# Performance work log

Hardware: AMD Instinct MI355X
Metric: run time of the kernel (lower is better)

## Reference

```python
import jax, jax.numpy as jnp
import numpy as np

SEQ_LENS = [1024, 768, 512, 896, 640, 384, 1024, 896]
TOTAL = sum(SEQ_LENS)  # 6144
EMBED = 768
NUM_HEADS = 12
HEAD_DIM = EMBED // NUM_HEADS
FFN = 3072
LN_EPS = 1e-5


def _pad_maps():
    # static (numpy) index maps for ragged <-> padded layout
    B, S = len(SEQ_LENS), max(SEQ_LENS)
    offs = np.cumsum([0] + SEQ_LENS)
    pad_idx = np.zeros((B, S), np.int32)
    valid = np.zeros((B, S), bool)
    for i, L in enumerate(SEQ_LENS):
        pad_idx[i, :L] = np.arange(offs[i], offs[i] + L)
        valid[i, :L] = True
    flat_b = np.concatenate([np.full(L, i, np.int32) for i, L in enumerate(SEQ_LENS)])
    flat_p = np.concatenate([np.arange(L, dtype=np.int32) for L in SEQ_LENS])
    return jnp.asarray(pad_idx), jnp.asarray(valid), jnp.asarray(flat_b), jnp.asarray(flat_p)

PAD_IDX, VALID, FLAT_B, FLAT_P = _pad_maps()


def _layernorm(x, g, b):
    mu = jnp.mean(x, axis=-1, keepdims=True)
    var = jnp.mean(jnp.square(x - mu), axis=-1, keepdims=True)
    return (x - mu) * jax.lax.rsqrt(var + LN_EPS) * g + b


def setup_inputs() -> dict:
    key = jax.random.key(0)
    ks = jax.random.split(key, 8)
    return {
        "hidden_states": jax.random.normal(ks[0], (TOTAL, EMBED), jnp.float32),
        "attention_mask": jnp.ones((TOTAL,), jnp.int32),
        "in_proj_w": 0.02 * jax.random.normal(ks[1], (3 * EMBED, EMBED), jnp.float32),
        "in_proj_b": jnp.zeros((3 * EMBED,), jnp.float32),
        "out_proj_w": 0.02 * jax.random.normal(ks[2], (EMBED, EMBED), jnp.float32),
        "out_proj_b": jnp.zeros((EMBED,), jnp.float32),
        "ln1_g": jnp.ones((EMBED,), jnp.float32),
        "ln1_b": jnp.zeros((EMBED,), jnp.float32),
        "fc1_w": 0.02 * jax.random.normal(ks[3], (FFN, EMBED), jnp.float32),
        "fc1_b": jnp.zeros((FFN,), jnp.float32),
        "fc2_w": 0.02 * jax.random.normal(ks[4], (EMBED, FFN), jnp.float32),
        "fc2_b": jnp.zeros((EMBED,), jnp.float32),
        "ln2_g": jnp.ones((EMBED,), jnp.float32),
        "ln2_b": jnp.zeros((EMBED,), jnp.float32),
    }


def reference(hidden_states, attention_mask, in_proj_w, in_proj_b, out_proj_w,
              out_proj_b, ln1_g, ln1_b, fc1_w, fc1_b, fc2_w, fc2_b, ln2_g, ln2_b):
    B, S = PAD_IDX.shape
    residual = hidden_states
    x = _layernorm(hidden_states, ln1_g, ln1_b)  # pre-LN (do_layer_norm_before)

    # ragged -> padded [B, S, E]; key validity combines padding mask and ragged tail
    xp = x[PAD_IDX]
    key_valid = VALID & (attention_mask[PAD_IDX] != 0)

    # fused QKV projection (nn.MultiheadAttention in_proj)
    qkv = xp @ in_proj_w.T + in_proj_b  # [B, S, 3E]
    q, k, v = jnp.split(qkv, 3, axis=-1)
    q = q.reshape(B, S, NUM_HEADS, HEAD_DIM) * (1.0 / np.sqrt(HEAD_DIM))
    k = k.reshape(B, S, NUM_HEADS, HEAD_DIM)
    v = v.reshape(B, S, NUM_HEADS, HEAD_DIM)

    scores = jnp.einsum('bqhd,bkhd->bhqk', q, k)  # [B, H, S, S]
    causal = jnp.tril(jnp.ones((S, S), bool))
    mask = causal[None, None] & key_valid[:, None, None, :]
    scores = jnp.where(mask, scores, jnp.float32(-1e30))
    probs = jax.nn.softmax(scores, axis=-1)
    ctx = jnp.einsum('bhqk,bkhd->bqhd', probs, v).reshape(B, S, EMBED)
    attn = ctx @ out_proj_w.T + out_proj_b

    # padded -> ragged, residual
    h = residual + attn[FLAT_B, FLAT_P]

    # FFN block (pre-LN)
    residual = h
    h = _layernorm(h, ln2_g, ln2_b)
    h = jax.nn.relu(h @ fc1_w.T + fc1_b)
    h = h @ fc2_w.T + fc2_b
    return residual + h
```

## Files before the change

### kernel.cpp

```cpp
#include <hip/hip_runtime.h>
#include <hip/hip_bf16.h>

#define TOTAL 6144
#define EMBED 768
#define QKV3  2304
#define FFN   3072
#define NH    12
#define HD    64
#define NSEG  412
#define NCQT  128
#define SLOTB 4608

typedef unsigned short u16;
typedef unsigned int u32;
typedef float f32x4 __attribute__((ext_vector_type(4)));
typedef __bf16 bf16x8 __attribute__((ext_vector_type(8)));

__device__ __constant__ int BOFF[9] = {0, 1024, 1792, 2304, 3200, 3840, 4224, 5248, 6144};

struct SegT {
    short segstart[193];
    short qt_of_seg[NSEG];
    short cqt[NCQT];
};
constexpr SegT make_segt() {
    SegT s{};
    const int toff[9] = {0, 32, 56, 72, 100, 120, 132, 164, 192};
    int tot = 0, cc = 0;
    for (int qt = 0; qt < 192; ++qt) {
        int b = 0;
        for (int i = 0; i < 8; ++i)
            if (qt >= toff[i + 1]) b = i + 1;
        int t = qt - toff[b];
        int nch = t / 2 + 1;
        int ns = (nch + 3) / 4;
        s.segstart[qt] = (short)tot;
        for (int j = 0; j < ns; ++j) s.qt_of_seg[tot + j] = (short)qt;
        tot += ns;
        if (ns >= 2) s.cqt[cc++] = (short)qt;
    }
    s.segstart[192] = (short)tot;
    return s;
}
__device__ __constant__ SegT SEGT = make_segt();

__device__ __forceinline__ u16 f2b(float f) {
    __bf16 h = (__bf16)f;
    return __builtin_bit_cast(u16, h);
}
__device__ __forceinline__ float b2f(u16 h) {
    union { u32 u; float f; } v; v.u = ((u32)h) << 16; return v.f;
}

__device__ __forceinline__ void gload_lds16(const u16* g, u16* l) {
    __builtin_amdgcn_global_load_lds(
        (const __attribute__((address_space(1))) u32*)(uintptr_t)g,
        (__attribute__((address_space(3))) u32*)(uintptr_t)l, 16, 0, 0);
}

__device__ __forceinline__ float rowmax16(float x) {
    int v;
    v = __builtin_amdgcn_mov_dpp(__float_as_int(x), 0xB1, 0xF, 0xF, true);
    x = fmaxf(x, __int_as_float(v));
    v = __builtin_amdgcn_mov_dpp(__float_as_int(x), 0x4E, 0xF, 0xF, true);
    x = fmaxf(x, __int_as_float(v));
    v = __builtin_amdgcn_mov_dpp(__float_as_int(x), 0x124, 0xF, 0xF, true);
    x = fmaxf(x, __int_as_float(v));
    v = __builtin_amdgcn_mov_dpp(__float_as_int(x), 0x128, 0xF, 0xF, true);
    x = fmaxf(x, __int_as_float(v));
    return x;
}

__global__ void cvt4m_kernel(const float* __restrict__ s0, u16* __restrict__ d0, int n0,
                             const float* __restrict__ s1, u16* __restrict__ d1, int n1,
                             const float* __restrict__ s2, u16* __restrict__ d2, int n2,
                             const float* __restrict__ s3, u16* __restrict__ d3, int n3,
                             const int* __restrict__ am, u32* __restrict__ mb) {
    if (blockIdx.x >= 6912) {
        int g = (blockIdx.x - 6912) * 4 + (threadIdx.x >> 6);
        int lane = threadIdx.x & 63;
        unsigned long long bal = __ballot(am[g * 64 + lane] != 0);
        if (lane == 0) {
            mb[g * 2] = (u32)bal;
            mb[g * 2 + 1] = (u32)(bal >> 32);
        }
        return;
    }
    int i = blockIdx.x * blockDim.x + threadIdx.x;
    const float* s;
    u16* d;
    int j = i;
    if (j < n0) { s = s0; d = d0; }
    else {
        j -= n0;
        if (j < n1) { s = s1; d = d1; }
        else {
            j -= n1;
            if (j < n2) { s = s2; d = d2; }
            else {
                j -= n2;
                if (j >= n3) return;
                s = s3; d = d3;
            }
        }
    }
    float4 v = ((const float4*)s)[j];
    ushort4 o;
    o.x = f2b(v.x); o.y = f2b(v.y); o.z = f2b(v.z); o.w = f2b(v.w);
    ((ushort4*)d)[j] = o;
}

__global__ __launch_bounds__(256) void ln_kernel(const float* __restrict__ x,
                                                 const float* __restrict__ g,
                                                 const float* __restrict__ b,
                                                 u16* __restrict__ out) {
    int row = blockIdx.x * 4 + (threadIdx.x >> 6);
    int lane = threadIdx.x & 63;
    const float* xr = x + (size_t)row * EMBED;
    float4 v[3];
    float s = 0.f, sq = 0.f;
#pragma unroll
    for (int c = 0; c < 3; ++c) {
        v[c] = *(const float4*)(xr + c * 256 + lane * 4);
        s += v[c].x + v[c].y + v[c].z + v[c].w;
        sq += v[c].x * v[c].x + v[c].y * v[c].y + v[c].z * v[c].z + v[c].w * v[c].w;
    }
#pragma unroll
    for (int o = 32; o; o >>= 1) {
        s += __shfl_xor(s, o);
        sq += __shfl_xor(sq, o);
    }
    float mu = s * (1.f / 768.f);
    float var = sq * (1.f / 768.f) - mu * mu;
    float rs = rsqrtf(var + 1e-5f);
    u16* orow = out + (size_t)row * EMBED;
#pragma unroll
    for (int c = 0; c < 3; ++c) {
        int col = c * 256 + lane * 4;
        float4 gg = *(const float4*)(g + col);
        float4 bb = *(const float4*)(b + col);
        ushort4 o;
        o.x = f2b((v[c].x - mu) * rs * gg.x + bb.x);
        o.y = f2b((v[c].y - mu) * rs * gg.y + bb.y);
        o.z = f2b((v[c].z - mu) * rs * gg.z + bb.z);
        o.w = f2b((v[c].w - mu) * rs * gg.w + bb.w);
        *(ushort4*)(orow + col) = o;
    }
}

template <int RELU, int RES, int OUTB, int OUTF, int VTR>
__global__ __launch_bounds__(256) void gemm128(const u16* __restrict__ A,
                                               const u16* __restrict__ B,
                                               const float* __restrict__ bias,
                                               const float* __restrict__ res,
                                               u16* __restrict__ outb,
                                               float* __restrict__ outf,
                                               u16* __restrict__ vout,
                                               int M, int N, int K) {
    __shared__ u16 As[2][128][64];
    __shared__ u16 Bs[2][128][64];
    int t = threadIdx.x;
    int lane = t & 63, w = t >> 6;
    int wr = w >> 1, wc = w & 1;
    int gx = gridDim.x;
    int nwg = gx * gridDim.y;
    int flat = blockIdx.y * gx + blockIdx.x;
    int swz = (flat & 7) * (nwg >> 3) + (flat >> 3);
    int m0 = (swz / gx) * 128, n0 = (swz % gx) * 128;
    int lr = lane >> 3;
    int lcg = (lane & 7) ^ (lr & 7);
    int c16 = lane & 15, hi = lane >> 4;

    f32x4 acc[4][4];
#pragma unroll
    for (int m = 0; m < 4; ++m)
#pragma unroll
        for (int n = 0; n < 4; ++n) acc[m][n] = (f32x4)0.f;

    const u16* Ab = A + (size_t)(m0 + w * 32 + lr) * K + lcg * 8;
    const u16* Bb = B + (size_t)(n0 + w * 32 + lr) * K + lcg * 8;

    int nk = K >> 6;
#pragma unroll
    for (int i = 0; i < 4; ++i) {
        gload_lds16(Ab + (size_t)(i * 8) * K, &As[0][w * 32 + i * 8][0]);
        gload_lds16(Bb + (size_t)(i * 8) * K, &Bs[0][w * 32 + i * 8][0]);
    }

    for (int tk = 0; tk < nk; ++tk) {
        int cur = tk & 1;
        if (tk + 1 < nk) {
            int k1 = (tk + 1) << 6;
#pragma unroll
            for (int i = 0; i < 4; ++i) {
                gload_lds16(Ab + (size_t)(i * 8) * K + k1, &As[cur ^ 1][w * 32 + i * 8][0]);
                gload_lds16(Bb + (size_t)(i * 8) * K + k1, &Bs[cur ^ 1][w * 32 + i * 8][0]);
            }
            asm volatile("s_waitcnt vmcnt(8)" ::: "memory");
        } else {
            asm volatile("s_waitcnt vmcnt(0)" ::: "memory");
        }
        __builtin_amdgcn_sched_barrier(0);
        __builtin_amdgcn_s_barrier();
#pragma unroll
        for (int ks = 0; ks < 2; ++ks) {
            bf16x8 af[4], bfr[4];
#pragma unroll
            for (int m = 0; m < 4; ++m)
                af[m] = *(const bf16x8*)&As[cur][wr * 64 + m * 16 + c16][((ks * 4 + hi) ^ (c16 & 7)) * 8];
#pragma unroll
            for (int n = 0; n < 4; ++n)
                bfr[n] = *(const bf16x8*)&Bs[cur][wc * 64 + n * 16 + c16][((ks * 4 + hi) ^ (c16 & 7)) * 8];
#pragma unroll
            for (int m = 0; m < 4; ++m)
#pragma unroll
                for (int n = 0; n < 4; ++n)
                    acc[m][n] = __builtin_amdgcn_mfma_f32_16x16x32_bf16(af[m], bfr[n], acc[m][n], 0, 0, 0);
        }
        asm volatile("s_waitcnt lgkmcnt(0)" ::: "memory");
        __builtin_amdgcn_sched_barrier(0);
        __builtin_amdgcn_s_barrier();
    }

#pragma unroll
    for (int m = 0; m < 4; ++m)
#pragma unroll
        for (int n = 0; n < 4; ++n) {
            int cg = n0 + wc * 64 + n * 16 + c16;
            float bv = bias[cg];
            float vj[4];
#pragma unroll
            for (int j = 0; j < 4; ++j) {
                int rg = m0 + wr * 64 + m * 16 + hi * 4 + j;
                float v = acc[m][n][j] + bv;
                if (RELU) v = fmaxf(v, 0.f);
                if (RES) v += res[(size_t)rg * N + cg];
                vj[j] = v;
                if (OUTB) outb[(size_t)rg * N + cg] = f2b(v);
                if (OUTF) outf[(size_t)rg * N + cg] = v;
            }
            if (VTR && cg >= 2 * EMBED) {
                ushort4 tv;
                tv.x = f2b(vj[0]); tv.y = f2b(vj[1]); tv.z = f2b(vj[2]); tv.w = f2b(vj[3]);
                int rgb = m0 + wr * 64 + m * 16 + hi * 4;
                *(ushort4*)&vout[(size_t)(cg - 2 * EMBED) * TOTAL + rgb] = tv;
            }
        }
}

__global__ __launch_bounds__(64, 2) void attn_mfma(const u16* __restrict__ qkv,
                                                   const u16* __restrict__ vT,
                                                   const u32* __restrict__ mbits,
                                                   u16* __restrict__ ctx,
                                                   char* __restrict__ pbuf) {
    __shared__ u16 Pl[32][64];
    int l = threadIdx.x;
    int hi = l >> 4, c = l & 15;
    int bidg = blockIdx.x;
    int swz = (bidg & 7) * (NSEG * NH / 8) + (bidg >> 3);
    int h = swz / NSEG;
    int sl = swz % NSEG;
    int qt = SEGT.qt_of_seg[sl];
    int seg = sl - SEGT.segstart[qt];
    int nseg = SEGT.segstart[qt + 1] - SEGT.segstart[qt];
    int r0 = qt * 32;
    int b = 0;
#pragma unroll
    for (int i = 0; i < 8; ++i)
        if (r0 >= BOFF[i + 1]) b = i + 1;
    int boff = BOFF[b];
    int p0 = r0 - boff;
    int nchunks = (p0 >> 6) + 1;
    int nfull = (p0 >= 63) ? (((p0 - 63) >> 6) + 1) : 0;
    int kc0 = seg * 4;
    int kc1 = min(kc0 + 4, nchunks);
    const float SCALE = 0.125f * 1.44269504f;

    bf16x8 qa[2][2];
#pragma unroll
    for (int m = 0; m < 2; ++m)
#pragma unroll
        for (int ks = 0; ks < 2; ++ks)
            qa[m][ks] = *(const bf16x8*)&qkv[(size_t)(r0 + m * 16 + c) * QKV3 + h * HD + ks * 32 + hi * 8];

    bf16x8 vones;
#pragma unroll
    for (int j = 0; j < 8; ++j) vones[j] = (__bf16)1.0f;

    f32x4 oacc[2][4], lacc[2];
    float mrun[2][4];
#pragma unroll
    for (int m = 0; m < 2; ++m) {
        lacc[m] = (f32x4)0.f;
#pragma unroll
        for (int nt = 0; nt < 4; ++nt) oacc[m][nt] = (f32x4)0.f;
#pragma unroll
        for (int r = 0; r < 4; ++r) mrun[m][r] = -1e30f;
    }

    for (int kc = kc0; kc < kc1; ++kc) {
        int k0 = kc << 6;
        bf16x8 kb[2][4], vb[2][4];
#pragma unroll
        for (int ks = 0; ks < 2; ++ks)
#pragma unroll
            for (int nt = 0; nt < 4; ++nt) {
                kb[ks][nt] = *(const bf16x8*)&qkv[(size_t)(boff + k0 + nt * 16 + c) * QKV3 +
                                                  EMBED + h * HD + ks * 32 + hi * 8];
                vb[ks][nt] = *(const bf16x8*)&vT[(size_t)(h * HD + nt * 16 + c) * TOTAL +
                                                 boff + k0 + ks * 32 + hi * 8];
            }
        int wi = (boff + k0) >> 5;
        u32 mw0 = mbits[wi], mw1 = mbits[wi + 1];

        f32x4 sacc[2][4];
#pragma unroll
        for (int m = 0; m < 2; ++m)
#pragma unroll
            for (int nt = 0; nt < 4; ++nt) sacc[m][nt] = (f32x4)0.f;
        __builtin_amdgcn_s_setprio(1);
#pragma unroll
        for (int ks = 0; ks < 2; ++ks)
#pragma unroll
            for (int m = 0; m < 2; ++m)
#pragma unroll
                for (int nt = 0; nt < 4; ++nt)
                    sacc[m][nt] = __builtin_amdgcn_mfma_f32_16x16x32_bf16(qa[m][ks], kb[ks][nt], sacc[m][nt], 0, 0, 0);
        __builtin_amdgcn_s_setprio(0);

        bool fullmask = ((mw0 & mw1) == 0xFFFFFFFFu);
        if (kc >= nfull) {
#pragma unroll
            for (int m = 0; m < 2; ++m)
#pragma unroll
                for (int nt = 0; nt < 4; ++nt) {
                    int kpos = k0 + nt * 16 + c;
                    u32 mwv = (nt & 2) ? mw1 : mw0;
                    float madd = fullmask ? 0.f
                        : (((mwv >> (((nt & 1) << 4) + c)) & 1u) ? 0.f : -1e30f);
#pragma unroll
                    for (int r = 0; r < 4; ++r) {
                        int qp = p0 + m * 16 + 4 * hi + r;
                        sacc[m][nt][r] = (kpos <= qp) ? (sacc[m][nt][r] + madd) : -1e30f;
                    }
                }
        } else if (!fullmask) {
#pragma unroll
            for (int m = 0; m < 2; ++m)
#pragma unroll
                for (int nt = 0; nt < 4; ++nt) {
                    u32 mwv = (nt & 2) ? mw1 : mw0;
                    float madd = ((mwv >> (((nt & 1) << 4) + c)) & 1u) ? 0.f : -1e30f;
#pragma unroll
                    for (int r = 0; r < 4; ++r) sacc[m][nt][r] += madd;
                }
        }

        float mx[2][4];
        int small = 1;
#pragma unroll
        for (int m = 0; m < 2; ++m)
#pragma unroll
            for (int r = 0; r < 4; ++r) {
                float v = fmaxf(fmaxf(sacc[m][0][r], sacc[m][1][r]),
                                fmaxf(sacc[m][2][r], sacc[m][3][r]));
                v = rowmax16(v);
                mx[m][r] = v;
                small &= (v <= mrun[m][r]) ? 1 : 0;
            }
        if (!__all(small)) {
#pragma unroll
            for (int m = 0; m < 2; ++m)
#pragma unroll
                for (int r = 0; r < 4; ++r) {
                    float mn = fmaxf(mrun[m][r], mx[m][r]);
                    float f = exp2f((mrun[m][r] - mn) * SCALE);
                    mrun[m][r] = mn;
                    lacc[m][r] *= f;
#pragma unroll
                    for (int nt = 0; nt < 4; ++nt) oacc[m][nt][r] *= f;
                }
        }

        float negm[2][4];
#pragma unroll
        for (int m = 0; m < 2; ++m)
#pragma unroll
            for (int r = 0; r < 4; ++r) negm[m][r] = -mrun[m][r] * SCALE;
#pragma unroll
        for (int m = 0; m < 2; ++m)
#pragma unroll
            for (int nt = 0; nt < 4; ++nt)
#pragma unroll
                for (int r = 0; r < 4; ++r) {
                    float p = exp2f(fmaf(sacc[m][nt][r], SCALE, negm[m][r]));
                    int row = m * 16 + 4 * hi + r;
                    int cch = ((nt * 2 + (c >> 3)) ^ (row & 7)) << 3;
                    Pl[row][cch + (c & 7)] = f2b(p);
                }

#pragma unroll
        for (int ks = 0; ks < 2; ++ks) {
            bf16x8 pa[2];
#pragma unroll
            for (int m = 0; m < 2; ++m)
                pa[m] = *(const bf16x8*)&Pl[m * 16 + c][(((ks * 4 + hi) ^ (c & 7)) << 3)];
            __builtin_amdgcn_s_setprio(1);
#pragma unroll
            for (int m = 0; m < 2; ++m) {
                lacc[m] = __builtin_amdgcn_mfma_f32_16x16x32_bf16(pa[m], vones, lacc[m], 0, 0, 0);
#pragma unroll
                for (int nt = 0; nt < 4; ++nt)
                    oacc[m][nt] = __builtin_amdgcn_mfma_f32_16x16x32_bf16(pa[m], vb[ks][nt], oacc[m][nt], 0, 0, 0);
            }
            __builtin_amdgcn_s_setprio(0);
        }
    }

    if (nseg == 1) {
#pragma unroll
        for (int m = 0; m < 2; ++m)
#pragma unroll
            for (int r = 0; r < 4; ++r) {
                float inv = 1.0f / lacc[m][r];
#pragma unroll
                for (int nt = 0; nt < 4; ++nt)
                    ctx[(size_t)(r0 + m * 16 + 4 * hi + r) * EMBED + h * HD + nt * 16 + c] =
                        f2b(oacc[m][nt][r] * inv);
            }
    } else {
        char* base = pbuf + (size_t)(h * NSEG + sl) * SLOTB;
        u16* Op = (u16*)base;
        float* mlp = (float*)(base + 4096);
#pragma unroll
        for (int m = 0; m < 2; ++m)
#pragma unroll
            for (int r = 0; r < 4; ++r) {
                int row = m * 16 + 4 * hi + r;
                float inv = 1.0f / lacc[m][r];
#pragma unroll
                for (int nt = 0; nt < 4; ++nt)
                    Op[row * 64 + nt * 16 + c] = f2b(oacc[m][nt][r] * inv);
                if (c == 0) {
                    mlp[row * 2] = mrun[m][r];
                    mlp[row * 2 + 1] = lacc[m][r];
                }
            }
    }
}

__global__ __launch_bounds__(256) void attn_combine(const char* __restrict__ pbuf,
                                                    u16* __restrict__ ctx) {
    int cid = blockIdx.x;
    int h = cid % NH;
    int qt = SEGT.cqt[cid / NH];
    int s0 = SEGT.segstart[qt];
    int ns = SEGT.segstart[qt + 1] - s0;
    int t = threadIdx.x;
    int r = t >> 3;
    int cg = t & 7;
    int r0 = qt * 32;
    const float SCALE = 0.125f * 1.44269504f;

    float mj[4], lj[4];
    uint4 ov[4];
#pragma unroll
    for (int j = 0; j < 4; ++j) {
        const char* base = pbuf + (size_t)(h * NSEG + s0 + min(j, ns - 1)) * SLOTB;
        float2 ml = *(const float2*)(base + 4096 + r * 8);
        mj[j] = (j < ns) ? ml.x : -1e30f;
        lj[j] = (j < ns) ? ml.y : 0.f;
        ov[j] = *(const uint4*)(base + (r * 64 + cg * 8) * 2);
    }
    float M = fmaxf(fmaxf(mj[0], mj[1]), fmaxf(mj[2], mj[3]));
    float e[4], wsum = 0.f;
#pragma unroll
    for (int j = 0; j < 4; ++j) {
        e[j] = (j < ns) ? exp2f((mj[j] - M) * SCALE) * lj[j] : 0.f;
        wsum += e[j];
    }
    float inv = 1.0f / wsum;
    u16 outv[8];
#pragma unroll
    for (int k = 0; k < 8; ++k) {
        float o = 0.f;
#pragma unroll
        for (int j = 0; j < 4; ++j)
            o += e[j] * b2f(((const u16*)&ov[j])[k]);
        outv[k] = f2b(o * inv);
    }
    *(uint4*)&ctx[(size_t)(r0 + r) * EMBED + h * HD + cg * 8] = *(uint4*)outv;
}

extern "C" void kernel_launch(void* const* d_in, const int* in_sizes, int n_in,
                              void* d_out, int out_size, void* d_ws, size_t ws_size,
                              hipStream_t stream) {
    (void)in_sizes; (void)n_in; (void)out_size; (void)ws_size;
    const float* hidden = (const float*)d_in[0];
    const int*   amask  = (const int*)d_in[1];
    const float* in_w   = (const float*)d_in[2];
    const float* in_b   = (const float*)d_in[3];
    const float* out_w  = (const float*)d_in[4];
    const float* out_b  = (const float*)d_in[5];
    const float* ln1g   = (const float*)d_in[6];
    const float* ln1b   = (const float*)d_in[7];
    const float* fc1w   = (const float*)d_in[8];
    const float* fc1b   = (const float*)d_in[9];
    const float* fc2w   = (const float*)d_in[10];
    const float* fc2b   = (const float*)d_in[11];
    const float* ln2g   = (const float*)d_in[12];
    const float* ln2b   = (const float*)d_in[13];
    float* out = (float*)d_out;

    char* ws = (char*)d_ws;
    size_t off = 0;
    auto alloc = [&](size_t bytes) {
        void* p = ws + off;
        off += (bytes + 255) & ~(size_t)255;
        return p;
    };
    u16* w_in_bf  = (u16*)alloc((size_t)QKV3 * EMBED * 2);
    u16* w_out_bf = (u16*)alloc((size_t)EMBED * EMBED * 2);
    u16* w_fc1_bf = (u16*)alloc((size_t)FFN * EMBED * 2);
    u16* w_fc2_bf = (u16*)alloc((size_t)EMBED * FFN * 2);
    u16* xln  = (u16*)alloc((size_t)TOTAL * EMBED * 2);
    u16* qkv  = (u16*)alloc((size_t)TOTAL * QKV3 * 2);
    u16* ctx  = (u16*)alloc((size_t)TOTAL * EMBED * 2);
    float* hmid = (float*)alloc((size_t)TOTAL * EMBED * 4);
    u16* hln  = (u16*)alloc((size_t)TOTAL * EMBED * 2);
    u16* f1o  = (u16*)alloc((size_t)TOTAL * FFN * 2);
    u32* mbits = (u32*)alloc(192 * 4);
    u16* vT = hln;
    char* pbuf = (char*)f1o;

    cvt4m_kernel<<<6936, 256, 0, stream>>>(in_w, w_in_bf, 442368,
                                           out_w, w_out_bf, 147456,
                                           fc1w, w_fc1_bf, 589824,
                                           fc2w, w_fc2_bf, 589824,
                                           amask, mbits);

    ln_kernel<<<TOTAL / 4, 256, 0, stream>>>(hidden, ln1g, ln1b, xln);
    gemm128<0, 0, 1, 0, 1><<<dim3(QKV3 / 128, TOTAL / 128), 256, 0, stream>>>(
        xln, w_in_bf, in_b, nullptr, qkv, nullptr, vT, TOTAL, QKV3, EMBED);
    attn_mfma<<<dim3(NSEG * NH), 64, 0, stream>>>(qkv, vT, mbits, ctx, pbuf);
    attn_combine<<<dim3(NCQT * NH), 256, 0, stream>>>(pbuf, ctx);
    gemm128<0, 1, 0, 1, 0><<<dim3(EMBED / 128, TOTAL / 128), 256, 0, stream>>>(
        ctx, w_out_bf, out_b, hidden, nullptr, hmid, nullptr, TOTAL, EMBED, EMBED);
    ln_kernel<<<TOTAL / 4, 256, 0, stream>>>(hmid, ln2g, ln2b, hln);
    gemm128<1, 0, 1, 0, 0><<<dim3(FFN / 128, TOTAL / 128), 256, 0, stream>>>(
        hln, w_fc1_bf, fc1b, nullptr, f1o, nullptr, nullptr, TOTAL, FFN, EMBED);
    gemm128<0, 1, 0, 1, 0><<<dim3(EMBED / 128, TOTAL / 128), 256, 0, stream>>>(
        f1o, w_fc2_bf, fc2b, hmid, nullptr, out, nullptr, TOTAL, EMBED, FFN);
}
```

Measured before the change: 214.6 us.

## Add 3-stage GEMM pipeline for FC2 and pack four attention segments per block

The GEMM gains a STAGES template parameter. A 3-deep LDS ring buffer with adjusted vmcnt waits is enabled only for the long-K FC2 projection, to hide more global-load latency. Separately, the attention kernel now runs four independent 64-lane segments per 256-thread workgroup, each with its own P tile in LDS, and uses a per-XCD block remapping. This cuts the number of workgroups, but raises LDS use per block. The FC2 occupancy may drop because the 3-stage buffers need 96KB of LDS per block.

```diff
diff --git a/kernel.cpp b/kernel.cpp
--- a/kernel.cpp
+++ b/kernel.cpp
@@ -148,7 +148,7 @@
     }
 }
 
-template <int RELU, int RES, int OUTB, int OUTF, int VTR>
+template <int RELU, int RES, int OUTB, int OUTF, int VTR, int STAGES>
 __global__ __launch_bounds__(256) void gemm128(const u16* __restrict__ A,
                                                const u16* __restrict__ B,
                                                const float* __restrict__ bias,
@@ -157,8 +157,8 @@
                                                float* __restrict__ outf,
                                                u16* __restrict__ vout,
                                                int M, int N, int K) {
-    __shared__ u16 As[2][128][64];
-    __shared__ u16 Bs[2][128][64];
+    __shared__ u16 As[STAGES][128][64];
+    __shared__ u16 Bs[STAGES][128][64];
     int t = threadIdx.x;
     int lane = t & 63, w = t >> 6;
     int wr = w >> 1, wc = w & 1;
@@ -181,24 +181,28 @@
     const u16* Bb = B + (size_t)(n0 + w * 32 + lr) * K + lcg * 8;
 
     int nk = K >> 6;
-#pragma unroll
-    for (int i = 0; i < 4; ++i) {
-        gload_lds16(Ab + (size_t)(i * 8) * K, &As[0][w * 32 + i * 8][0]);
-        gload_lds16(Bb + (size_t)(i * 8) * K, &Bs[0][w * 32 + i * 8][0]);
-    }
+    auto issue = [&](int tk, int buf) {
+        int k0 = tk << 6;
+#pragma unroll
+        for (int i = 0; i < 4; ++i) {
+            gload_lds16(Ab + (size_t)(i * 8) * K + k0, &As[buf][w * 32 + i * 8][0]);
+            gload_lds16(Bb + (size_t)(i * 8) * K + k0, &Bs[buf][w * 32 + i * 8][0]);
+        }
+    };
+    issue(0, 0);
+    if (STAGES == 3 && nk > 1) issue(1, 1);
 
     for (int tk = 0; tk < nk; ++tk) {
-        int cur = tk & 1;
-        if (tk + 1 < nk) {
-            int k1 = (tk + 1) << 6;
-#pragma unroll
-            for (int i = 0; i < 4; ++i) {
-                gload_lds16(Ab + (size_t)(i * 8) * K + k1, &As[cur ^ 1][w * 32 + i * 8][0]);
-                gload_lds16(Bb + (size_t)(i * 8) * K + k1, &Bs[cur ^ 1][w * 32 + i * 8][0]);
-            }
-            asm volatile("s_waitcnt vmcnt(8)" ::: "memory");
+        int cur = (STAGES == 2) ? (tk & 1) : (tk % 3);
+        if (tk + STAGES - 1 < nk)
+            issue(tk + STAGES - 1, (STAGES == 2) ? (cur ^ 1) : ((tk + 2) % 3));
+        if (STAGES == 3) {
+            if (tk + 2 < nk)      asm volatile("s_waitcnt vmcnt(16)" ::: "memory");
+            else if (tk + 1 < nk) asm volatile("s_waitcnt vmcnt(8)" ::: "memory");
+            else                  asm volatile("s_waitcnt vmcnt(0)" ::: "memory");
         } else {
-            asm volatile("s_waitcnt vmcnt(0)" ::: "memory");
+            if (tk + 1 < nk)      asm volatile("s_waitcnt vmcnt(8)" ::: "memory");
+            else                  asm volatile("s_waitcnt vmcnt(0)" ::: "memory");
         }
         __builtin_amdgcn_sched_barrier(0);
         __builtin_amdgcn_s_barrier();
@@ -248,18 +252,21 @@
         }
 }
 
-__global__ __launch_bounds__(64, 2) void attn_mfma(const u16* __restrict__ qkv,
-                                                   const u16* __restrict__ vT,
-                                                   const u32* __restrict__ mbits,
-                                                   u16* __restrict__ ctx,
-                                                   char* __restrict__ pbuf) {
-    __shared__ u16 Pl[32][64];
-    int l = threadIdx.x;
+__global__ __launch_bounds__(256) void attn_mfma(const u16* __restrict__ qkv,
+                                                 const u16* __restrict__ vT,
+                                                 const u32* __restrict__ mbits,
+                                                 u16* __restrict__ ctx,
+                                                 char* __restrict__ pbuf) {
+    __shared__ u16 Pl[4][32][64];
+    int l = threadIdx.x & 63, w = threadIdx.x >> 6;
     int hi = l >> 4, c = l & 15;
-    int bidg = blockIdx.x;
-    int swz = (bidg & 7) * (NSEG * NH / 8) + (bidg >> 3);
-    int h = swz / NSEG;
-    int sl = swz % NSEG;
+    int bid = blockIdx.x;
+    int xcd = bid & 7;
+    int base = (xcd < 4) ? xcd * 155 : 4 * 155 + (xcd - 4) * 154;
+    int wgid = base + (bid >> 3);
+    int sidx = wgid * 4 + w;
+    int h = sidx / NSEG;
+    int sl = sidx % NSEG;
     int qt = SEGT.qt_of_seg[sl];
     int seg = sl - SEGT.segstart[qt];
     int nseg = SEGT.segstart[qt + 1] - SEGT.segstart[qt];
@@ -396,7 +403,7 @@
                     float p = exp2f(fmaf(sacc[m][nt][r], SCALE, negm[m][r]));
                     int row = m * 16 + 4 * hi + r;
                     int cch = ((nt * 2 + (c >> 3)) ^ (row & 7)) << 3;
-                    Pl[row][cch + (c & 7)] = f2b(p);
+                    Pl[w][row][cch + (c & 7)] = f2b(p);
                 }
 
 #pragma unroll
@@ -404,7 +411,7 @@
             bf16x8 pa[2];
 #pragma unroll
             for (int m = 0; m < 2; ++m)
-                pa[m] = *(const bf16x8*)&Pl[m * 16 + c][(((ks * 4 + hi) ^ (c & 7)) << 3)];
+                pa[m] = *(const bf16x8*)&Pl[w][m * 16 + c][(((ks * 4 + hi) ^ (c & 7)) << 3)];
             __builtin_amdgcn_s_setprio(1);
 #pragma unroll
             for (int m = 0; m < 2; ++m) {
@@ -429,9 +436,9 @@
                         f2b(oacc[m][nt][r] * inv);
             }
     } else {
-        char* base = pbuf + (size_t)(h * NSEG + sl) * SLOTB;
-        u16* Op = (u16*)base;
-        float* mlp = (float*)(base + 4096);
+        char* base2 = pbuf + (size_t)(h * NSEG + sl) * SLOTB;
+        u16* Op = (u16*)base2;
+        float* mlp = (float*)(base2 + 4096);
 #pragma unroll
         for (int m = 0; m < 2; ++m)
 #pragma unroll
@@ -540,15 +547,15 @@
                                            amask, mbits);
 
     ln_kernel<<<TOTAL / 4, 256, 0, stream>>>(hidden, ln1g, ln1b, xln);
-    gemm128<0, 0, 1, 0, 1><<<dim3(QKV3 / 128, TOTAL / 128), 256, 0, stream>>>(
+    gemm128<0, 0, 1, 0, 1, 2><<<dim3(QKV3 / 128, TOTAL / 128), 256, 0, stream>>>(
         xln, w_in_bf, in_b, nullptr, qkv, nullptr, vT, TOTAL, QKV3, EMBED);
-    attn_mfma<<<dim3(NSEG * NH), 64, 0, stream>>>(qkv, vT, mbits, ctx, pbuf);
+    attn_mfma<<<dim3(NSEG * NH / 4), 256, 0, stream>>>(qkv, vT, mbits, ctx, pbuf);
     attn_combine<<<dim3(NCQT * NH), 256, 0, stream>>>(pbuf, ctx);
-    gemm128<0, 1, 0, 1, 0><<<dim3(EMBED / 128, TOTAL / 128), 256, 0, stream>>>(
+    gemm128<0, 1, 0, 1, 0, 2><<<dim3(EMBED / 128, TOTAL / 128), 256, 0, stream>>>(
         ctx, w_out_bf, out_b, hidden, nullptr, hmid, nullptr, TOTAL, EMBED, EMBED);
     ln_kernel<<<TOTAL / 4, 256, 0, stream>>>(hmid, ln2g, ln2b, hln);
-    gemm128<1, 0, 1, 0, 0><<<dim3(FFN / 128, TOTAL / 128), 256, 0, stream>>>(
+    gemm128<1, 0, 1, 0, 0, 2><<<dim3(FFN / 128, TOTAL / 128), 256, 0, stream>>>(
         hln, w_fc1_bf, fc1b, nullptr, f1o, nullptr, nullptr, TOTAL, FFN, EMBED);
-    gemm128<0, 1, 0, 1, 0><<<dim3(EMBED / 128, TOTAL / 128), 256, 0, stream>>>(
+    gemm128<0, 1, 0, 1, 0, 3><<<dim3(EMBED / 128, TOTAL / 128), 256, 0, stream>>>(
         f1o, w_fc2_bf, fc2b, hmid, nullptr, out, nullptr, TOTAL, EMBED, FFN);
 }
```

New measurement: 270.9 us. +26.3%, slower.

## Split FC2 GEMM K dimension in two with separate partial-sum add kernel

Applied to the files above, without the earlier changes.

The FC2 GEMM is launched with twice the workgroups, each covering half of K. The second half writes raw partial sums into the dead qkv buffer, and a new elementwise kernel adds them into the output. This targets the poor wave fill of the 288-block grid on a 256-CU device, at the cost of an extra fp32 write/read pass and one more kernel launch.

```diff
diff --git a/kernel.cpp b/kernel.cpp
--- a/kernel.cpp
+++ b/kernel.cpp
@@ -148,7 +148,7 @@
     }
 }
 
-template <int RELU, int RES, int OUTB, int OUTF, int VTR>
+template <int RELU, int RES, int OUTB, int OUTF, int VTR, int SPLITK>
 __global__ __launch_bounds__(256) void gemm128(const u16* __restrict__ A,
                                                const u16* __restrict__ B,
                                                const float* __restrict__ bias,
@@ -156,6 +156,7 @@
                                                u16* __restrict__ outb,
                                                float* __restrict__ outf,
                                                u16* __restrict__ vout,
+                                               float* __restrict__ outf2,
                                                int M, int N, int K) {
     __shared__ u16 As[2][128][64];
     __shared__ u16 Bs[2][128][64];
@@ -166,7 +167,12 @@
     int nwg = gx * gridDim.y;
     int flat = blockIdx.y * gx + blockIdx.x;
     int swz = (flat & 7) * (nwg >> 3) + (flat >> 3);
-    int m0 = (swz / gx) * 128, n0 = (swz % gx) * 128;
+    int cx = swz % gx;
+    int nxt = gx / SPLITK;
+    int kh = (SPLITK > 1) ? (cx / nxt) : 0;
+    int n0 = (cx % nxt) * 128;
+    int m0 = (swz / gx) * 128;
+    int Ksub = K / SPLITK;
     int lr = lane >> 3;
     int lcg = (lane & 7) ^ (lr & 7);
     int c16 = lane & 15, hi = lane >> 4;
@@ -177,10 +183,10 @@
 #pragma unroll
         for (int n = 0; n < 4; ++n) acc[m][n] = (f32x4)0.f;
 
-    const u16* Ab = A + (size_t)(m0 + w * 32 + lr) * K + lcg * 8;
-    const u16* Bb = B + (size_t)(n0 + w * 32 + lr) * K + lcg * 8;
-
-    int nk = K >> 6;
+    const u16* Ab = A + (size_t)(m0 + w * 32 + lr) * K + kh * Ksub + lcg * 8;
+    const u16* Bb = B + (size_t)(n0 + w * 32 + lr) * K + kh * Ksub + lcg * 8;
+
+    int nk = Ksub >> 6;
 #pragma unroll
     for (int i = 0; i < 4; ++i) {
         gload_lds16(Ab + (size_t)(i * 8) * K, &As[0][w * 32 + i * 8][0]);
@@ -232,6 +238,10 @@
 #pragma unroll
             for (int j = 0; j < 4; ++j) {
                 int rg = m0 + wr * 64 + m * 16 + hi * 4 + j;
+                if (SPLITK > 1 && kh == 1) {
+                    outf2[(size_t)rg * N + cg] = acc[m][n][j];
+                    continue;
+                }
                 float v = acc[m][n][j] + bv;
                 if (RELU) v = fmaxf(v, 0.f);
                 if (RES) v += res[(size_t)rg * N + cg];
@@ -246,6 +256,17 @@
                 *(ushort4*)&vout[(size_t)(cg - 2 * EMBED) * TOTAL + rgb] = tv;
             }
         }
+}
+
+__global__ __launch_bounds__(256) void addbuf_kernel(float* __restrict__ out,
+                                                     const float* __restrict__ p1, int n4) {
+    int i = blockIdx.x * blockDim.x + threadIdx.x;
+    if (i < n4) {
+        float4 a = ((const float4*)out)[i];
+        float4 b = ((const float4*)p1)[i];
+        a.x += b.x; a.y += b.y; a.z += b.z; a.w += b.w;
+        ((float4*)out)[i] = a;
+    }
 }
 
 __global__ __launch_bounds__(64, 2) void attn_mfma(const u16* __restrict__ qkv,
@@ -532,6 +553,7 @@
     u32* mbits = (u32*)alloc(192 * 4);
     u16* vT = hln;
     char* pbuf = (char*)f1o;
+    float* fc2p1 = (float*)qkv;
 
     cvt4m_kernel<<<6936, 256, 0, stream>>>(in_w, w_in_bf, 442368,
                                            out_w, w_out_bf, 147456,
@@ -540,15 +562,17 @@
                                            amask, mbits);
 
     ln_kernel<<<TOTAL / 4, 256, 0, stream>>>(hidden, ln1g, ln1b, xln);
-    gemm128<0, 0, 1, 0, 1><<<dim3(QKV3 / 128, TOTAL / 128), 256, 0, stream>>>(
-        xln, w_in_bf, in_b, nullptr, qkv, nullptr, vT, TOTAL, QKV3, EMBED);
+    gemm128<0, 0, 1, 0, 1, 1><<<dim3(QKV3 / 128, TOTAL / 128), 256, 0, stream>>>(
+        xln, w_in_bf, in_b, nullptr, qkv, nullptr, vT, nullptr, TOTAL, QKV3, EMBED);
     attn_mfma<<<dim3(NSEG * NH), 64, 0, stream>>>(qkv, vT, mbits, ctx, pbuf);
     attn_combine<<<dim3(NCQT * NH), 256, 0, stream>>>(pbuf, ctx);
-    gemm128<0, 1, 0, 1, 0><<<dim3(EMBED / 128, TOTAL / 128), 256, 0, stream>>>(
-        ctx, w_out_bf, out_b, hidden, nullptr, hmid, nullptr, TOTAL, EMBED, EMBED);
+    gemm128<0, 1, 0, 1, 0, 1><<<dim3(EMBED / 128, TOTAL / 128), 256, 0, stream>>>(
+        ctx, w_out_bf, out_b, hidden, nullptr, hmid, nullptr, nullptr, TOTAL, EMBED, EMBED);
     ln_kernel<<<TOTAL / 4, 256, 0, stream>>>(hmid, ln2g, ln2b, hln);
-    gemm128<1, 0, 1, 0, 0><<<dim3(FFN / 128, TOTAL / 128), 256, 0, stream>>>(
-        hln, w_fc1_bf, fc1b, nullptr, f1o, nullptr, nullptr, TOTAL, FFN, EMBED);
-    gemm128<0, 1, 0, 1, 0><<<dim3(EMBED / 128, TOTAL / 128), 256, 0, stream>>>(
-        f1o, w_fc2_bf, fc2b, hmid, nullptr, out, nullptr, TOTAL, EMBED, FFN);
-}
+    gemm128<1, 0, 1, 0, 0, 1><<<dim3(FFN / 128, TOTAL / 128), 256, 0, stream>>>(
+        hln, w_fc1_bf, fc1b, nullptr, f1o, nullptr, nullptr, nullptr, TOTAL, FFN, EMBED);
+    gemm128<0, 1, 0, 1, 0, 2><<<dim3(2 * EMBED / 128, TOTAL / 128), 256, 0, stream>>>(
+        f1o, w_fc2_bf, fc2b, hmid, nullptr, out, nullptr, fc2p1, TOTAL, EMBED, FFN);
+    addbuf_kernel<<<(TOTAL * EMBED / 4 + 255) / 256, 256, 0, stream>>>(
+        out, fc2p1, TOTAL * EMBED / 4);
+}
```

After: 237.5 us. 1.11x slower.
